# Performance work log

Measured on AMD Instinct MI355X. Metric: run time of the kernel, lower is better.

Reference implementation:

```python
import jax, jax.numpy as jnp
import numpy as np


def setup_inputs() -> dict:
    key = jax.random.key(0)
    ks = jax.random.split(key, 7)
    B, D, N, R = 256, 5120, 16, 160  # batch, d_inner, d_state, dt_rank
    x = jax.random.normal(ks[0], (B, D), jnp.float32)
    h0 = jax.random.normal(ks[1], (B, D, N), jnp.float32)
    W_x_dt = jax.random.normal(ks[2], (D, R), jnp.float32) * (1.0 / np.sqrt(D))
    W_dt = jax.random.normal(ks[3], (R, D), jnp.float32) * (1.0 / np.sqrt(R))
    b_dt = jax.random.normal(ks[4], (D,), jnp.float32)
    W_BC = jax.random.normal(ks[5], (D, 2 * N), jnp.float32) * (1.0 / np.sqrt(D))
    A_log = jax.random.normal(ks[6], (D, N), jnp.float32)
    return {"x": x, "h0": h0, "W_x_dt": W_x_dt, "W_dt": W_dt,
            "b_dt": b_dt, "W_BC": W_BC, "A_log": A_log}


def reference(x, h0, W_x_dt, W_dt, b_dt, W_BC, A_log):
    # Single-token Mamba selective SSM step (batch dims squeezed: x [B,D], h0 [B,D,N]).
    N = A_log.shape[1]
    # delta_t = softplus(dt_proj(delta_t_proj(x)))  -> [B, D]
    dt = jax.nn.softplus((x @ W_x_dt) @ W_dt + b_dt)
    # BC projection, split into B and C parts -> [B, N] each
    BC = x @ W_BC
    Bm, Cm = BC[:, :N], BC[:, N:]
    A = -jnp.exp(A_log)                              # [D, N]
    delta_A = jnp.exp(A[None, :, :] * dt[:, :, None])   # [B, D, N]
    delta_Bx = (dt * x)[:, :, None] * Bm[:, None, :]     # [B, D, N]
    h = delta_A * h0 + delta_Bx                          # new hidden state
    # y = h @ C (per-batch bmm over state dim) + x residual
    y = jnp.einsum('bdn,bn->bd', h, Cm) + x              # [B, D]
    return y
```

## Files before the change

kernel.cpp:

```cpp
#include <hip/hip_runtime.h>
#include <math.h>

#define BB 256
#define DD 5120
#define NN 16
#define RR 160
#define CT 192
#define NSPLIT 32
#define TMP_ELEMS (BB * CT)
#define NEGA_ELEMS (DD * NN)

__global__ __launch_bounds__(256) void k1_gemm(const float* __restrict__ x,
                                               const float* __restrict__ Wxdt,
                                               const float* __restrict__ Wbc,
                                               float* __restrict__ part) {
    __shared__ float xs[32][68];
    __shared__ float ws[32][64];
    const int tid = threadIdx.x;
    const int tx = tid & 15, ty = tid >> 4;
    const int c0 = blockIdx.x * 64;
    const int b0 = blockIdx.y * 64;
    const int k0 = blockIdx.z * 160;
    float acc[4][4] = {};

    for (int kc = 0; kc < 160; kc += 32) {
        {
            const int i  = tid >> 3;
            const int j4 = (tid & 7) * 4;
            #pragma unroll
            for (int rep = 0; rep < 2; ++rep) {
                const int row = i + rep * 32;
                const float4 v = *(const float4*)&x[(size_t)(b0 + row) * DD + k0 + kc + j4];
                xs[j4 + 0][row] = v.x;
                xs[j4 + 1][row] = v.y;
                xs[j4 + 2][row] = v.z;
                xs[j4 + 3][row] = v.w;
            }
        }
        {
            const int c4 = (tid & 15) * 4;
            const int r0 = tid >> 4;
            #pragma unroll
            for (int rep = 0; rep < 2; ++rep) {
                const int r  = r0 + rep * 16;
                const int kg = k0 + kc + r;
                const int cg = c0 + c4;
                float4 v;
                if (cg < RR) v = *(const float4*)&Wxdt[(size_t)kg * RR + cg];
                else         v = *(const float4*)&Wbc[(size_t)kg * 32 + (cg - RR)];
                *(float4*)&ws[r][c4] = v;
            }
        }
        __syncthreads();
        #pragma unroll
        for (int k = 0; k < 32; ++k) {
            const float4 a4 = *(const float4*)&xs[k][ty * 4];
            const float4 w4 = *(const float4*)&ws[k][tx * 4];
            const float av[4] = {a4.x, a4.y, a4.z, a4.w};
            const float wv[4] = {w4.x, w4.y, w4.z, w4.w};
            #pragma unroll
            for (int u = 0; u < 4; ++u)
                #pragma unroll
                for (int v = 0; v < 4; ++v)
                    acc[u][v] = fmaf(av[u], wv[v], acc[u][v]);
        }
        __syncthreads();
    }

    float* p = part + (size_t)blockIdx.z * TMP_ELEMS;
    #pragma unroll
    for (int u = 0; u < 4; ++u) {
        const int b = b0 + ty * 4 + u;
        *(float4*)&p[b * CT + c0 + tx * 4] =
            make_float4(acc[u][0], acc[u][1], acc[u][2], acc[u][3]);
    }
}

__global__ __launch_bounds__(256) void k_red(const float* __restrict__ part,
                                             const float* __restrict__ Alog,
                                             float* __restrict__ tmp,
                                             float* __restrict__ negA) {
    const int idx = blockIdx.x * 256 + threadIdx.x;
    if (idx < TMP_ELEMS) {
        float s = 0.f;
        #pragma unroll
        for (int z = 0; z < NSPLIT; ++z) s += part[(size_t)z * TMP_ELEMS + idx];
        tmp[idx] = s;
    } else {
        const int j = idx - TMP_ELEMS;
        negA[j] = -__expf(Alog[j]);
    }
}

__global__ __launch_bounds__(256) void k2_dt(const float* __restrict__ tmp,
                                             const float* __restrict__ Wdt,
                                             const float* __restrict__ bdt,
                                             float* __restrict__ dt) {
    __shared__ float ts[32][34];
    __shared__ float ws[32][64];
    const int tid = threadIdx.x;
    const int tx = tid & 15, ty = tid >> 4;
    const int d0 = blockIdx.x * 64;
    const int b0 = blockIdx.y * 32;
    float acc[2][4] = {};

    for (int kc = 0; kc < RR; kc += 32) {
        {
            const int row = tid >> 3;
            const int j4  = (tid & 7) * 4;
            const float4 v = *(const float4*)&tmp[(size_t)(b0 + row) * CT + kc + j4];
            ts[j4 + 0][row] = v.x;
            ts[j4 + 1][row] = v.y;
            ts[j4 + 2][row] = v.z;
            ts[j4 + 3][row] = v.w;
        }
        {
            const int c4 = (tid & 15) * 4;
            const int r0 = tid >> 4;
            #pragma unroll
            for (int rep = 0; rep < 2; ++rep) {
                const int r = r0 + rep * 16;
                *(float4*)&ws[r][c4] = *(const float4*)&Wdt[(size_t)(kc + r) * DD + d0 + c4];
            }
        }
        __syncthreads();
        #pragma unroll
        for (int k = 0; k < 32; ++k) {
            const float a0 = ts[k][ty * 2 + 0];
            const float a1 = ts[k][ty * 2 + 1];
            const float4 w4 = *(const float4*)&ws[k][tx * 4];
            const float wv[4] = {w4.x, w4.y, w4.z, w4.w};
            #pragma unroll
            for (int v = 0; v < 4; ++v) {
                acc[0][v] = fmaf(a0, wv[v], acc[0][v]);
                acc[1][v] = fmaf(a1, wv[v], acc[1][v]);
            }
        }
        __syncthreads();
    }

    const float4 bv = *(const float4*)&bdt[d0 + tx * 4];
    const float bb[4] = {bv.x, bv.y, bv.z, bv.w};
    #pragma unroll
    for (int u = 0; u < 2; ++u) {
        const int b = b0 + ty * 2 + u;
        float o[4];
        #pragma unroll
        for (int v = 0; v < 4; ++v) {
            const float z = acc[u][v] + bb[v];
            o[v] = fmaxf(z, 0.f) + log1pf(__expf(-fabsf(z)));
        }
        *(float4*)&dt[(size_t)b * DD + d0 + tx * 4] = make_float4(o[0], o[1], o[2], o[3]);
    }
}

__global__ __launch_bounds__(256) void k3_ssm(const float* __restrict__ x,
                                              const float* __restrict__ h0,
                                              const float* __restrict__ dt,
                                              const float* __restrict__ tmp,
                                              const float* __restrict__ negA,
                                              float* __restrict__ out) {
    const int t  = blockIdx.x * 256 + threadIdx.x;
    const int b  = t / (DD / 4);
    const int dq = t - b * (DD / 4);
    const size_t base = (size_t)b * DD + dq * 4;

    const float4 xv  = *(const float4*)&x[base];
    const float4 dtv = *(const float4*)&dt[base];
    const float xs[4]  = {xv.x, xv.y, xv.z, xv.w};
    const float dts[4] = {dtv.x, dtv.y, dtv.z, dtv.w};

    const float* bc = &tmp[(size_t)b * CT + RR];
    float bm[16], cm[16];
    #pragma unroll
    for (int q4 = 0; q4 < 4; ++q4) {
        const float4 v = *(const float4*)&bc[q4 * 4];
        bm[q4 * 4 + 0] = v.x; bm[q4 * 4 + 1] = v.y; bm[q4 * 4 + 2] = v.z; bm[q4 * 4 + 3] = v.w;
        const float4 w = *(const float4*)&bc[16 + q4 * 4];
        cm[q4 * 4 + 0] = w.x; cm[q4 * 4 + 1] = w.y; cm[q4 * 4 + 2] = w.z; cm[q4 * 4 + 3] = w.w;
    }

    float y[4];
    #pragma unroll
    for (int j = 0; j < 4; ++j) {
        const int d = dq * 4 + j;
        const float dtj = dts[j];
        const float dtx = dtj * xs[j];
        const float* hp = &h0[(base + j) * NN];
        const float* ap = &negA[(size_t)d * NN];
        float acc = xs[j];
        #pragma unroll
        for (int q4 = 0; q4 < 4; ++q4) {
            const float4 a4 = *(const float4*)&ap[q4 * 4];
            const float4 h4 = *(const float4*)&hp[q4 * 4];
            const float av[4] = {a4.x, a4.y, a4.z, a4.w};
            const float hv[4] = {h4.x, h4.y, h4.z, h4.w};
            #pragma unroll
            for (int q = 0; q < 4; ++q) {
                const int n = q4 * 4 + q;
                const float dA = __expf(av[q] * dtj);
                const float h  = fmaf(dA, hv[q], dtx * bm[n]);
                acc = fmaf(h, cm[n], acc);
            }
        }
        y[j] = acc;
    }
    *(float4*)&out[base] = make_float4(y[0], y[1], y[2], y[3]);
}

extern "C" void kernel_launch(void* const* d_in, const int* in_sizes, int n_in,
                              void* d_out, int out_size, void* d_ws, size_t ws_size,
                              hipStream_t stream) {
    const float* x    = (const float*)d_in[0];
    const float* h0   = (const float*)d_in[1];
    const float* Wxdt = (const float*)d_in[2];
    const float* Wdt  = (const float*)d_in[3];
    const float* bdt  = (const float*)d_in[4];
    const float* Wbc  = (const float*)d_in[5];
    const float* Alog = (const float*)d_in[6];
    float* out = (float*)d_out;

    float* part  = (float*)d_ws;
    float* tmp   = part + (size_t)NSPLIT * TMP_ELEMS;
    float* negA  = tmp + TMP_ELEMS;
    float* dtbuf = negA + NEGA_ELEMS;

    k1_gemm<<<dim3(3, 4, NSPLIT), 256, 0, stream>>>(x, Wxdt, Wbc, part);
    k_red<<<dim3((TMP_ELEMS + NEGA_ELEMS) / 256), 256, 0, stream>>>(part, Alog, tmp, negA);
    k2_dt<<<dim3(DD / 64, BB / 32), 256, 0, stream>>>(tmp, Wdt, bdt, dtbuf);
    k3_ssm<<<dim3((BB * DD / 4) / 256), 256, 0, stream>>>(x, h0, dtbuf, tmp, negA, out);
}
```

Before: 190.1 us.

## Fuse dt projection GEMM with SSM state update into one kernel

Merges the dt projection/softplus kernel with the SSM update kernel. dt is now computed in registers and used directly, so the intermediate dt buffer is never written to or read back from global memory, and one launch is removed. negA and the B/C rows are staged in shared memory per block. The trade-off is that the h0-streaming phase runs on fewer blocks (640 instead of 1280) and sits behind the GEMM loop, which may reduce memory-level parallelism.

```diff
diff --git a/kernel.cpp b/kernel.cpp
--- a/kernel.cpp
+++ b/kernel.cpp
@@ -92,18 +92,38 @@
     }
 }
 
-__global__ __launch_bounds__(256) void k2_dt(const float* __restrict__ tmp,
-                                             const float* __restrict__ Wdt,
-                                             const float* __restrict__ bdt,
-                                             float* __restrict__ dt) {
+__global__ __launch_bounds__(256) void k23_fused(const float* __restrict__ x,
+                                                 const float* __restrict__ h0,
+                                                 const float* __restrict__ Wdt,
+                                                 const float* __restrict__ bdt,
+                                                 const float* __restrict__ tmp,
+                                                 const float* __restrict__ negA,
+                                                 float* __restrict__ out) {
     __shared__ float ts[32][34];
     __shared__ float ws[32][64];
+    __shared__ float As[64][17];
+    __shared__ float BCs[32][33];
     const int tid = threadIdx.x;
     const int tx = tid & 15, ty = tid >> 4;
     const int d0 = blockIdx.x * 64;
     const int b0 = blockIdx.y * 32;
+
+    {
+        const int i  = tid >> 2;
+        const int n4 = (tid & 3) * 4;
+        const float4 v = *(const float4*)&negA[(size_t)(d0 + i) * NN + n4];
+        As[i][n4 + 0] = v.x; As[i][n4 + 1] = v.y;
+        As[i][n4 + 2] = v.z; As[i][n4 + 3] = v.w;
+    }
+    {
+        const int row = tid >> 3;
+        const int c4  = (tid & 7) * 4;
+        const float4 v = *(const float4*)&tmp[(size_t)(b0 + row) * CT + RR + c4];
+        BCs[row][c4 + 0] = v.x; BCs[row][c4 + 1] = v.y;
+        BCs[row][c4 + 2] = v.z; BCs[row][c4 + 3] = v.w;
+    }
+
     float acc[2][4] = {};
-
     for (int kc = 0; kc < RR; kc += 32) {
         {
             const int row = tid >> 3;
@@ -141,71 +161,43 @@
 
     const float4 bv = *(const float4*)&bdt[d0 + tx * 4];
     const float bb[4] = {bv.x, bv.y, bv.z, bv.w};
+
     #pragma unroll
     for (int u = 0; u < 2; ++u) {
         const int b = b0 + ty * 2 + u;
-        float o[4];
+        const size_t base = (size_t)b * DD + d0 + tx * 4;
+        const float4 xv = *(const float4*)&x[base];
+        const float xs4[4] = {xv.x, xv.y, xv.z, xv.w};
+        const float* bm = &BCs[ty * 2 + u][0];
+        const float* cm = &BCs[ty * 2 + u][16];
+        float y[4];
         #pragma unroll
         for (int v = 0; v < 4; ++v) {
-            const float z = acc[u][v] + bb[v];
-            o[v] = fmaxf(z, 0.f) + log1pf(__expf(-fabsf(z)));
-        }
-        *(float4*)&dt[(size_t)b * DD + d0 + tx * 4] = make_float4(o[0], o[1], o[2], o[3]);
-    }
-}
-
-__global__ __launch_bounds__(256) void k3_ssm(const float* __restrict__ x,
-                                              const float* __restrict__ h0,
-                                              const float* __restrict__ dt,
-                                              const float* __restrict__ tmp,
-                                              const float* __restrict__ negA,
-                                              float* __restrict__ out) {
-    const int t  = blockIdx.x * 256 + threadIdx.x;
-    const int b  = t / (DD / 4);
-    const int dq = t - b * (DD / 4);
-    const size_t base = (size_t)b * DD + dq * 4;
-
-    const float4 xv  = *(const float4*)&x[base];
-    const float4 dtv = *(const float4*)&dt[base];
-    const float xs[4]  = {xv.x, xv.y, xv.z, xv.w};
-    const float dts[4] = {dtv.x, dtv.y, dtv.z, dtv.w};
-
-    const float* bc = &tmp[(size_t)b * CT + RR];
-    float bm[16], cm[16];
-    #pragma unroll
-    for (int q4 = 0; q4 < 4; ++q4) {
-        const float4 v = *(const float4*)&bc[q4 * 4];
-        bm[q4 * 4 + 0] = v.x; bm[q4 * 4 + 1] = v.y; bm[q4 * 4 + 2] = v.z; bm[q4 * 4 + 3] = v.w;
-        const float4 w = *(const float4*)&bc[16 + q4 * 4];
-        cm[q4 * 4 + 0] = w.x; cm[q4 * 4 + 1] = w.y; cm[q4 * 4 + 2] = w.z; cm[q4 * 4 + 3] = w.w;
-    }
-
-    float y[4];
-    #pragma unroll
-    for (int j = 0; j < 4; ++j) {
-        const int d = dq * 4 + j;
-        const float dtj = dts[j];
-        const float dtx = dtj * xs[j];
-        const float* hp = &h0[(base + j) * NN];
-        const float* ap = &negA[(size_t)d * NN];
-        float acc = xs[j];
-        #pragma unroll
-        for (int q4 = 0; q4 < 4; ++q4) {
-            const float4 a4 = *(const float4*)&ap[q4 * 4];
-            const float4 h4 = *(const float4*)&hp[q4 * 4];
-            const float av[4] = {a4.x, a4.y, a4.z, a4.w};
-            const float hv[4] = {h4.x, h4.y, h4.z, h4.w};
-            #pragma unroll
-            for (int q = 0; q < 4; ++q) {
-                const int n = q4 * 4 + q;
-                const float dA = __expf(av[q] * dtj);
-                const float h  = fmaf(dA, hv[q], dtx * bm[n]);
-                acc = fmaf(h, cm[n], acc);
-            }
-        }
-        y[j] = acc;
-    }
-    *(float4*)&out[base] = make_float4(y[0], y[1], y[2], y[3]);
+            const int dsub = tx * 4 + v;
+            const float z  = acc[u][v] + bb[v];
+            const float dt = fmaxf(z, 0.f) + log1pf(__expf(-fabsf(z)));
+            const float xe = xs4[v];
+            const float dtx = dt * xe;
+            const float* hp = &h0[(base + (size_t)v) * NN];
+            float acc_y = xe;
+            #pragma unroll
+            for (int n4 = 0; n4 < NN; n4 += 4) {
+                const float4 a4 = *(const float4*)&As[dsub][n4];
+                const float4 h4 = *(const float4*)&hp[n4];
+                const float av[4] = {a4.x, a4.y, a4.z, a4.w};
+                const float hv[4] = {h4.x, h4.y, h4.z, h4.w};
+                #pragma unroll
+                for (int q = 0; q < 4; ++q) {
+                    const int n = n4 + q;
+                    const float dA = __expf(av[q] * dt);
+                    const float h  = fmaf(dA, hv[q], dtx * bm[n]);
+                    acc_y = fmaf(h, cm[n], acc_y);
+                }
+            }
+            y[v] = acc_y;
+        }
+        *(float4*)&out[base] = make_float4(y[0], y[1], y[2], y[3]);
+    }
 }
 
 extern "C" void kernel_launch(void* const* d_in, const int* in_sizes, int n_in,
@@ -220,13 +212,11 @@
     const float* Alog = (const float*)d_in[6];
     float* out = (float*)d_out;
 
-    float* part  = (float*)d_ws;
-    float* tmp   = part + (size_t)NSPLIT * TMP_ELEMS;
-    float* negA  = tmp + TMP_ELEMS;
-    float* dtbuf = negA + NEGA_ELEMS;
+    float* part = (float*)d_ws;
+    float* tmp  = part + (size_t)NSPLIT * TMP_ELEMS;
+    float* negA = tmp + TMP_ELEMS;
 
     k1_gemm<<<dim3(3, 4, NSPLIT), 256, 0, stream>>>(x, Wxdt, Wbc, part);
     k_red<<<dim3((TMP_ELEMS + NEGA_ELEMS) / 256), 256, 0, stream>>>(part, Alog, tmp, negA);
-    k2_dt<<<dim3(DD / 64, BB / 32), 256, 0, stream>>>(tmp, Wdt, bdt, dtbuf);
-    k3_ssm<<<dim3((BB * DD / 4) / 256), 256, 0, stream>>>(x, h0, dtbuf, tmp, negA, out);
-}
+    k23_fused<<<dim3(DD / 64, BB / 32), 256, 0, stream>>>(x, h0, Wdt, bdt, tmp, negA, out);
+}
```

Result: faster. 185.7 us (-2.3%).

## Double split-K in projection GEMM and remap SSM kernel to two channels per thread

Applied to the files above, without the earlier changes.

The projection GEMM now splits K into 64 chunks of 80 instead of 32 chunks of 160, using 16-wide k tiles, so it launches twice as many blocks across the GPU. The cost is twice as much partial-sum traffic for the reduction kernel to read back. The SSM kernel now gives each thread 2 channels instead of 4 on a 2D grid with one batch row per block y. B and C are staged through shared memory, all h0 and negA loads are issued up front, and the C-dot uses two accumulators for more ILP. The intent is better occupancy and memory-level parallelism in the bandwidth-bound h0 stream.

```diff
diff --git a/kernel.cpp b/kernel.cpp
--- a/kernel.cpp
+++ b/kernel.cpp
@@ -6,7 +6,8 @@
 #define NN 16
 #define RR 160
 #define CT 192
-#define NSPLIT 32
+#define NSPLIT 64
+#define KSPL 80
 #define TMP_ELEMS (BB * CT)
 #define NEGA_ELEMS (DD * NN)
 
@@ -14,46 +15,38 @@
                                                const float* __restrict__ Wxdt,
                                                const float* __restrict__ Wbc,
                                                float* __restrict__ part) {
-    __shared__ float xs[32][68];
-    __shared__ float ws[32][64];
+    __shared__ float xs[16][68];
+    __shared__ float ws[16][64];
     const int tid = threadIdx.x;
     const int tx = tid & 15, ty = tid >> 4;
     const int c0 = blockIdx.x * 64;
     const int b0 = blockIdx.y * 64;
-    const int k0 = blockIdx.z * 160;
+    const int k0 = blockIdx.z * KSPL;
     float acc[4][4] = {};
 
-    for (int kc = 0; kc < 160; kc += 32) {
-        {
-            const int i  = tid >> 3;
-            const int j4 = (tid & 7) * 4;
-            #pragma unroll
-            for (int rep = 0; rep < 2; ++rep) {
-                const int row = i + rep * 32;
-                const float4 v = *(const float4*)&x[(size_t)(b0 + row) * DD + k0 + kc + j4];
-                xs[j4 + 0][row] = v.x;
-                xs[j4 + 1][row] = v.y;
-                xs[j4 + 2][row] = v.z;
-                xs[j4 + 3][row] = v.w;
-            }
-        }
-        {
+    for (int kc = 0; kc < KSPL; kc += 16) {
+        {
+            const int row = tid >> 2;
+            const int j4  = (tid & 3) * 4;
+            const float4 v = *(const float4*)&x[(size_t)(b0 + row) * DD + k0 + kc + j4];
+            xs[j4 + 0][row] = v.x;
+            xs[j4 + 1][row] = v.y;
+            xs[j4 + 2][row] = v.z;
+            xs[j4 + 3][row] = v.w;
+        }
+        {
+            const int r  = tid >> 4;
             const int c4 = (tid & 15) * 4;
-            const int r0 = tid >> 4;
-            #pragma unroll
-            for (int rep = 0; rep < 2; ++rep) {
-                const int r  = r0 + rep * 16;
-                const int kg = k0 + kc + r;
-                const int cg = c0 + c4;
-                float4 v;
-                if (cg < RR) v = *(const float4*)&Wxdt[(size_t)kg * RR + cg];
-                else         v = *(const float4*)&Wbc[(size_t)kg * 32 + (cg - RR)];
-                *(float4*)&ws[r][c4] = v;
-            }
-        }
-        __syncthreads();
-        #pragma unroll
-        for (int k = 0; k < 32; ++k) {
+            const int kg = k0 + kc + r;
+            const int cg = c0 + c4;
+            float4 v;
+            if (cg < RR) v = *(const float4*)&Wxdt[(size_t)kg * RR + cg];
+            else         v = *(const float4*)&Wbc[(size_t)kg * 32 + (cg - RR)];
+            *(float4*)&ws[r][c4] = v;
+        }
+        __syncthreads();
+        #pragma unroll
+        for (int k = 0; k < 16; ++k) {
             const float4 a4 = *(const float4*)&xs[k][ty * 4];
             const float4 w4 = *(const float4*)&ws[k][tx * 4];
             const float av[4] = {a4.x, a4.y, a4.z, a4.w};
@@ -160,52 +153,57 @@
                                               const float* __restrict__ tmp,
                                               const float* __restrict__ negA,
                                               float* __restrict__ out) {
-    const int t  = blockIdx.x * 256 + threadIdx.x;
-    const int b  = t / (DD / 4);
-    const int dq = t - b * (DD / 4);
-    const size_t base = (size_t)b * DD + dq * 4;
-
-    const float4 xv  = *(const float4*)&x[base];
-    const float4 dtv = *(const float4*)&dt[base];
-    const float xs[4]  = {xv.x, xv.y, xv.z, xv.w};
-    const float dts[4] = {dtv.x, dtv.y, dtv.z, dtv.w};
-
-    const float* bc = &tmp[(size_t)b * CT + RR];
-    float bm[16], cm[16];
+    __shared__ float bcS[32];
+    const int tid = threadIdx.x;
+    const int b   = blockIdx.y;
+    const int d2  = blockIdx.x * 512 + tid * 2;
+    const size_t base = (size_t)b * DD + d2;
+
+    if (tid < 32) bcS[tid] = tmp[(size_t)b * CT + RR + tid];
+    __syncthreads();
+
+    const float2 xe  = *(const float2*)&x[base];
+    const float2 dtv = *(const float2*)&dt[base];
+    const float* hp = &h0[base * NN];
+    float4 ha[4], hb[4];
+    #pragma unroll
+    for (int i = 0; i < 4; ++i) ha[i] = *(const float4*)&hp[i * 4];
+    #pragma unroll
+    for (int i = 0; i < 4; ++i) hb[i] = *(const float4*)&hp[NN + i * 4];
+    const float* ap = &negA[(size_t)d2 * NN];
+    float4 na0[4], na1[4];
+    #pragma unroll
+    for (int i = 0; i < 4; ++i) na0[i] = *(const float4*)&ap[i * 4];
+    #pragma unroll
+    for (int i = 0; i < 4; ++i) na1[i] = *(const float4*)&ap[NN + i * 4];
+
+    const float dt0 = dtv.x, dt1 = dtv.y;
+    const float dtx0 = dt0 * xe.x;
+    const float dtx1 = dt1 * xe.y;
+
+    float bm[NN], cm[NN];
+    #pragma unroll
+    for (int n = 0; n < NN; ++n) { bm[n] = bcS[n]; cm[n] = bcS[16 + n]; }
+
+    float y0a = xe.x, y0b = 0.f, y1a = xe.y, y1b = 0.f;
     #pragma unroll
     for (int q4 = 0; q4 < 4; ++q4) {
-        const float4 v = *(const float4*)&bc[q4 * 4];
-        bm[q4 * 4 + 0] = v.x; bm[q4 * 4 + 1] = v.y; bm[q4 * 4 + 2] = v.z; bm[q4 * 4 + 3] = v.w;
-        const float4 w = *(const float4*)&bc[16 + q4 * 4];
-        cm[q4 * 4 + 0] = w.x; cm[q4 * 4 + 1] = w.y; cm[q4 * 4 + 2] = w.z; cm[q4 * 4 + 3] = w.w;
-    }
-
-    float y[4];
-    #pragma unroll
-    for (int j = 0; j < 4; ++j) {
-        const int d = dq * 4 + j;
-        const float dtj = dts[j];
-        const float dtx = dtj * xs[j];
-        const float* hp = &h0[(base + j) * NN];
-        const float* ap = &negA[(size_t)d * NN];
-        float acc = xs[j];
-        #pragma unroll
-        for (int q4 = 0; q4 < 4; ++q4) {
-            const float4 a4 = *(const float4*)&ap[q4 * 4];
-            const float4 h4 = *(const float4*)&hp[q4 * 4];
-            const float av[4] = {a4.x, a4.y, a4.z, a4.w};
-            const float hv[4] = {h4.x, h4.y, h4.z, h4.w};
-            #pragma unroll
-            for (int q = 0; q < 4; ++q) {
-                const int n = q4 * 4 + q;
-                const float dA = __expf(av[q] * dtj);
-                const float h  = fmaf(dA, hv[q], dtx * bm[n]);
-                acc = fmaf(h, cm[n], acc);
-            }
-        }
-        y[j] = acc;
-    }
-    *(float4*)&out[base] = make_float4(y[0], y[1], y[2], y[3]);
+        const float av0[4] = {na0[q4].x, na0[q4].y, na0[q4].z, na0[q4].w};
+        const float av1[4] = {na1[q4].x, na1[q4].y, na1[q4].z, na1[q4].w};
+        const float hv0[4] = {ha[q4].x, ha[q4].y, ha[q4].z, ha[q4].w};
+        const float hv1[4] = {hb[q4].x, hb[q4].y, hb[q4].z, hb[q4].w};
+        #pragma unroll
+        for (int q = 0; q < 4; ++q) {
+            const int n = q4 * 4 + q;
+            const float dA0 = __expf(av0[q] * dt0);
+            const float h00 = fmaf(dA0, hv0[q], dtx0 * bm[n]);
+            const float dA1 = __expf(av1[q] * dt1);
+            const float h11 = fmaf(dA1, hv1[q], dtx1 * bm[n]);
+            if (n & 1) { y0b = fmaf(h00, cm[n], y0b); y1b = fmaf(h11, cm[n], y1b); }
+            else       { y0a = fmaf(h00, cm[n], y0a); y1a = fmaf(h11, cm[n], y1a); }
+        }
+    }
+    *(float2*)&out[base] = make_float2(y0a + y0b, y1a + y1b);
 }
 
 extern "C" void kernel_launch(void* const* d_in, const int* in_sizes, int n_in,
@@ -228,5 +226,5 @@
     k1_gemm<<<dim3(3, 4, NSPLIT), 256, 0, stream>>>(x, Wxdt, Wbc, part);
     k_red<<<dim3((TMP_ELEMS + NEGA_ELEMS) / 256), 256, 0, stream>>>(part, Alog, tmp, negA);
     k2_dt<<<dim3(DD / 64, BB / 32), 256, 0, stream>>>(tmp, Wdt, bdt, dtbuf);
-    k3_ssm<<<dim3((BB * DD / 4) / 256), 256, 0, stream>>>(x, h0, dtbuf, tmp, negA, out);
-}
+    k3_ssm<<<dim3(10, BB), 256, 0, stream>>>(x, h0, dtbuf, tmp, negA, out);
+}
```

After: 197.3 us. 3.8% more time.
